# Performance work log

Hardware: AMD Instinct MI355X
Metric: run time of the kernel (lower is better)

## Reference

```python
import jax, jax.numpy as jnp
import numpy as np
from jax import lax


def setup_inputs() -> dict:
    key = jax.random.key(0)
    ks = jax.random.split(key, 6)
    num_u, num_v, num_h, batch = 64, 256, 256, 8192
    # lecun_normal: std = 1/sqrt(fan_in) where fan_in is the last dim
    def lecun(k, shape):
        return jax.random.normal(k, shape, dtype=jnp.float32) * jnp.sqrt(1.0 / shape[1])
    return {
        "u_state": (jax.random.uniform(ks[0], (batch, num_u)) < 0.5).astype(jnp.float32),
        "weights_vu": lecun(ks[1], (num_v, num_u)),
        "weights_hu": lecun(ks[2], (num_h, num_u)),
        "weights_hv": lecun(ks[3], (num_h, num_v)),
        "bias_v": jax.random.normal(ks[4], (num_v,), dtype=jnp.float32) * 0.01,
        "bias_h": jax.random.normal(ks[5], (num_h,), dtype=jnp.float32) * 0.01,
        "therm_steps": 24,
        "size": 8,
    }


def reference(u_state, weights_vu, weights_hu, weights_hv, bias_v, bias_h,
              therm_steps, size):
    """ConditionalRBM.sample: init visible from u, thermalize therm_steps
    Gibbs sweeps, then collect `size` consecutive Gibbs samples."""
    key = jax.random.key(1)

    def bern(k, p):
        # binomial(n=1, p) == bernoulli(p)
        return (jax.random.uniform(k, p.shape) < p).astype(jnp.float32)

    def gibbs_step(v, k):
        k1, k2 = jax.random.split(k)
        ph = jax.nn.sigmoid(v @ weights_hv.T + u_state @ weights_hu.T + bias_h)  # [B,H]
        h = bern(k1, ph)
        pv = jax.nn.sigmoid(h @ weights_hv + u_state @ weights_vu.T + bias_v)    # [B,V]
        return bern(k2, pv)

    ks = jax.random.split(key, therm_steps + size + 1)
    # initial visible state from the conditional prior p(v|u)
    v0 = bern(ks[0], jax.nn.sigmoid(u_state @ weights_vu.T + bias_v))
    # thermalization chain (sequential, loop-carried)
    v_therm, _ = lax.scan(lambda v, k: (gibbs_step(v, k), None), v0, ks[1:1 + therm_steps])
    # sampling chain, stack the `size` samples
    def sample_step(v, k):
        v_new = gibbs_step(v, k)
        return v_new, v_new
    _, samples = lax.scan(sample_step, v_therm, ks[1 + therm_steps:])
    return samples.astype(jnp.uint8)  # [size, B, V]
```

## Files before the change

### kernel.cpp

```cpp
#include <hip/hip_runtime.h>
#include <cstdint>
#include <cstddef>


#pragma clang fp contract(off)

#define BATCH 8192
#define NU 64
#define NF 256
#define BM 64
#define BN 64
#define RTI 16
#define THERM 24
#define NSAMP 8

__host__ __device__ __forceinline__ void tf2x32(uint32_t k0, uint32_t k1,
                                                uint32_t x0, uint32_t x1,
                                                uint32_t* o0, uint32_t* o1) {
  uint32_t ks2 = k0 ^ k1 ^ 0x1BD11BDAu;
  x0 += k0; x1 += k1;
#define TFR(r) { x0 += x1; x1 = (x1 << (r)) | (x1 >> (32 - (r))); x1 ^= x0; }
  TFR(13) TFR(15) TFR(26) TFR(6)
  x0 += k1;  x1 += ks2 + 1u;
  TFR(17) TFR(29) TFR(16) TFR(24)
  x0 += ks2; x1 += k0 + 2u;
  TFR(13) TFR(15) TFR(26) TFR(6)
  x0 += k0;  x1 += k1 + 3u;
  TFR(17) TFR(29) TFR(16) TFR(24)
  x0 += k1;  x1 += ks2 + 4u;
  TFR(13) TFR(15) TFR(26) TFR(6)
  x0 += ks2; x1 += k0 + 5u;
#undef TFR
  *o0 = x0; *o1 = x1;
}

__device__ __forceinline__ float xla_expf(float x) {
  float xc = fminf(x, 88.3762626647950f);
  xc = fmaxf(xc, -88.3762626647949f);
  float fx = floorf(__builtin_fmaf(xc, 1.44269504088896341f, 0.5f));
  float tmp = 0.693359375f * fx;
  float z = -2.12194440e-4f * fx;
  float r = xc - tmp;
  r = r - z;
  z = r * r;
  float y = __builtin_fmaf(r, 1.9875691500e-4f, 1.3981999507e-3f);
  y = __builtin_fmaf(y, r, 8.3334519073e-3f);
  y = __builtin_fmaf(y, r, 4.1665795894e-2f);
  y = __builtin_fmaf(y, r, 1.6666665459e-1f);
  y = __builtin_fmaf(y, r, 5.0000001201e-1f);
  y = __builtin_fmaf(y, z, r);
  y = y + 1.0f;
  int n = (int)fx;
  float p2 = __int_as_float((n + 127) << 23);
  float res = y * p2;
  return fmaxf(res, x);
}

__device__ __forceinline__ float sigmoid_ref(float x) {
  float e = xla_expf(-x);
  return 1.0f / (1.0f + e);
}

__device__ __forceinline__ float bern_sample(uint32_t key0, uint32_t key1,
                                             uint32_t idx, float p) {
  uint32_t b0, b1;
  tf2x32(key0, key1, 0u, idx, &b0, &b1);
  uint32_t bits = b0 ^ b1;
  float u = __uint_as_float((bits >> 9) | 0x3f800000u) - 1.0f;
  return (u < p) ? 1.0f : 0.0f;
}

__global__ void k_transpose(const float* __restrict__ Whv,
                            float* __restrict__ WhvT) {
  int j = threadIdx.x;
  int k = blockIdx.x;
  WhvT[k * NF + j] = Whv[j * NF + k];
}

__global__ __launch_bounds__(256, 2) void k_udot(const float* __restrict__ U,
                                                 const float* __restrict__ W,
                                                 float* __restrict__ out) {
  __shared__ __align__(16) float Ulds[NU * RTI];
  const int j = threadIdx.x;
  const int i0 = blockIdx.x * RTI;
  const int si = j & 15;
  const int sg = j >> 4;
  {
    float4 u4 = *(const float4*)(U + (size_t)(i0 + si) * NU + sg * 4);
    Ulds[(sg * 4 + 0) * RTI + si] = u4.x;
    Ulds[(sg * 4 + 1) * RTI + si] = u4.y;
    Ulds[(sg * 4 + 2) * RTI + si] = u4.z;
    Ulds[(sg * 4 + 3) * RTI + si] = u4.w;
  }
  float wreg[NU];
  const float4* wr4 = (const float4*)(W + (size_t)j * NU);
#pragma unroll
  for (int r = 0; r < NU / 4; ++r) {
    float4 t = wr4[r];
    wreg[4 * r + 0] = t.x; wreg[4 * r + 1] = t.y;
    wreg[4 * r + 2] = t.z; wreg[4 * r + 3] = t.w;
  }
  __syncthreads();
  float acc[RTI];
#pragma unroll
  for (int i = 0; i < RTI; ++i) acc[i] = 0.0f;
#pragma unroll
  for (int kk = 0; kk < NU; ++kk) {
    const float w = wreg[kk];
    const float4 s0 = *(const float4*)(&Ulds[kk * RTI + 0]);
    const float4 s1 = *(const float4*)(&Ulds[kk * RTI + 4]);
    const float4 s2 = *(const float4*)(&Ulds[kk * RTI + 8]);
    const float4 s3 = *(const float4*)(&Ulds[kk * RTI + 12]);
    acc[0]  = __builtin_fmaf(s0.x, w, acc[0]);
    acc[1]  = __builtin_fmaf(s0.y, w, acc[1]);
    acc[2]  = __builtin_fmaf(s0.z, w, acc[2]);
    acc[3]  = __builtin_fmaf(s0.w, w, acc[3]);
    acc[4]  = __builtin_fmaf(s1.x, w, acc[4]);
    acc[5]  = __builtin_fmaf(s1.y, w, acc[5]);
    acc[6]  = __builtin_fmaf(s1.z, w, acc[6]);
    acc[7]  = __builtin_fmaf(s1.w, w, acc[7]);
    acc[8]  = __builtin_fmaf(s2.x, w, acc[8]);
    acc[9]  = __builtin_fmaf(s2.y, w, acc[9]);
    acc[10] = __builtin_fmaf(s2.z, w, acc[10]);
    acc[11] = __builtin_fmaf(s2.w, w, acc[11]);
    acc[12] = __builtin_fmaf(s3.x, w, acc[12]);
    acc[13] = __builtin_fmaf(s3.y, w, acc[13]);
    acc[14] = __builtin_fmaf(s3.z, w, acc[14]);
    acc[15] = __builtin_fmaf(s3.w, w, acc[15]);
  }
#pragma unroll
  for (int i = 0; i < RTI; ++i)
    out[(size_t)(i0 + i) * NF + j] = acc[i];
}

__global__ __launch_bounds__(256) void k_init(const float* __restrict__ uv,
                                              const float* __restrict__ bv,
                                              uint32_t* __restrict__ Vb,
                                              uint32_t key0, uint32_t key1) {
  const int j = threadIdx.x;
  const int i0 = blockIdx.x * RTI;
  const int wv = j >> 6, lane = j & 63;
  const float b = bv[j];
#pragma unroll
  for (int i = 0; i < RTI; ++i) {
    const int row = i0 + i;
    const uint32_t idx = (uint32_t)(row * NF + j);
    const float p = sigmoid_ref(uv[idx] + b);
    const float v = bern_sample(key0, key1, idx, p);
    unsigned long long m = __ballot(v != 0.0f);
    if (lane == 0)
      *(uint2*)(Vb + (size_t)row * 8 + 2 * wv) =
          make_uint2((uint32_t)m, (uint32_t)(m >> 32));
  }
}

__global__ __launch_bounds__(256, 2) void k_phase(
    const uint32_t* __restrict__ Sb, const float* __restrict__ W,
    const float* __restrict__ C, const float* __restrict__ bias,
    uint32_t* __restrict__ Ob, int* __restrict__ smp,
    uint32_t key0, uint32_t key1) {
  __shared__ __align__(16) float Wlds[NF * BN];
  __shared__ __align__(8) uint32_t Smask[BM * 8];
  __shared__ uint32_t Nib[BM * 16];
  const int t  = threadIdx.x;
  const int i0 = (blockIdx.x & 127) * BM;
  const int c0 = (blockIdx.x >> 7) * BN;
  const int rg = t >> 4, cg = t & 15;
  const int jc = c0 + cg * 4;
  const int r0 = i0 + rg * 4;

  {
    const int row = t >> 2, wo = (t & 3) * 2;
    *(uint2*)(&Smask[row * 8 + wo]) =
        *(const uint2*)(Sb + (size_t)(i0 + row) * 8 + wo);
  }
#pragma unroll
  for (int b = 0; b < 4; ++b) {
    float4 tmp0, tmp1, tmp2, tmp3;
    {
      const int f0 = (b * 4 + 0) * 256 + t;
      const int f1 = (b * 4 + 1) * 256 + t;
      const int f2 = (b * 4 + 2) * 256 + t;
      const int f3 = (b * 4 + 3) * 256 + t;
      tmp0 = *(const float4*)(W + (size_t)(f0 >> 4) * NF + c0 + (f0 & 15) * 4);
      tmp1 = *(const float4*)(W + (size_t)(f1 >> 4) * NF + c0 + (f1 & 15) * 4);
      tmp2 = *(const float4*)(W + (size_t)(f2 >> 4) * NF + c0 + (f2 & 15) * 4);
      tmp3 = *(const float4*)(W + (size_t)(f3 >> 4) * NF + c0 + (f3 & 15) * 4);
      *(float4*)(&Wlds[(size_t)(f0 >> 4) * BN + (f0 & 15) * 4]) = tmp0;
      *(float4*)(&Wlds[(size_t)(f1 >> 4) * BN + (f1 & 15) * 4]) = tmp1;
      *(float4*)(&Wlds[(size_t)(f2 >> 4) * BN + (f2 & 15) * 4]) = tmp2;
      *(float4*)(&Wlds[(size_t)(f3 >> 4) * BN + (f3 & 15) * 4]) = tmp3;
    }
  }
  __syncthreads();

  float acc[16];
#pragma unroll
  for (int q = 0; q < 16; ++q) acc[q] = 0.0f;

  const uint32_t* smrow = &Smask[(rg * 4) * 8];

  for (int wi = 0; wi < 8; ++wi) {
    const uint32_t wd0 = smrow[0 * 8 + wi];
    const uint32_t wd1 = smrow[1 * 8 + wi];
    const uint32_t wd2 = smrow[2 * 8 + wi];
    const uint32_t wd3 = smrow[3 * 8 + wi];
    const float* wl = &Wlds[(wi * 32) * BN + cg * 4];
#pragma unroll
    for (int kk = 0; kk < 32; ++kk) {
      const float4 w = *(const float4*)(wl + kk * BN);
      const float s0 = (float)((wd0 >> kk) & 1u);
      const float s1 = (float)((wd1 >> kk) & 1u);
      const float s2 = (float)((wd2 >> kk) & 1u);
      const float s3 = (float)((wd3 >> kk) & 1u);
      acc[0]  = __builtin_fmaf(s0, w.x, acc[0]);
      acc[1]  = __builtin_fmaf(s0, w.y, acc[1]);
      acc[2]  = __builtin_fmaf(s0, w.z, acc[2]);
      acc[3]  = __builtin_fmaf(s0, w.w, acc[3]);
      acc[4]  = __builtin_fmaf(s1, w.x, acc[4]);
      acc[5]  = __builtin_fmaf(s1, w.y, acc[5]);
      acc[6]  = __builtin_fmaf(s1, w.z, acc[6]);
      acc[7]  = __builtin_fmaf(s1, w.w, acc[7]);
      acc[8]  = __builtin_fmaf(s2, w.x, acc[8]);
      acc[9]  = __builtin_fmaf(s2, w.y, acc[9]);
      acc[10] = __builtin_fmaf(s2, w.z, acc[10]);
      acc[11] = __builtin_fmaf(s2, w.w, acc[11]);
      acc[12] = __builtin_fmaf(s3, w.x, acc[12]);
      acc[13] = __builtin_fmaf(s3, w.y, acc[13]);
      acc[14] = __builtin_fmaf(s3, w.z, acc[14]);
      acc[15] = __builtin_fmaf(s3, w.w, acc[15]);
    }
  }

  const float4 b4 = *(const float4*)(bias + jc);
  float vals[16];
#pragma unroll
  for (int ri = 0; ri < 4; ++ri) {
    const int row = r0 + ri;
    const float4 c4 = *(const float4*)(C + (size_t)row * NF + jc);
    const uint32_t idx0 = (uint32_t)(row * NF + jc);
    vals[ri * 4 + 0] = bern_sample(key0, key1, idx0 + 0,
        sigmoid_ref((acc[ri * 4 + 0] + c4.x) + b4.x));
    vals[ri * 4 + 1] = bern_sample(key0, key1, idx0 + 1,
        sigmoid_ref((acc[ri * 4 + 1] + c4.y) + b4.y));
    vals[ri * 4 + 2] = bern_sample(key0, key1, idx0 + 2,
        sigmoid_ref((acc[ri * 4 + 2] + c4.z) + b4.z));
    vals[ri * 4 + 3] = bern_sample(key0, key1, idx0 + 3,
        sigmoid_ref((acc[ri * 4 + 3] + c4.w) + b4.w));
  }

  if (smp) {
#pragma unroll
    for (int ri = 0; ri < 4; ++ri) {
      const int row = r0 + ri;
      int4 o;
      o.x = (vals[ri * 4 + 0] != 0.0f) ? 1 : 0;
      o.y = (vals[ri * 4 + 1] != 0.0f) ? 1 : 0;
      o.z = (vals[ri * 4 + 2] != 0.0f) ? 1 : 0;
      o.w = (vals[ri * 4 + 3] != 0.0f) ? 1 : 0;
      *(int4*)(smp + (size_t)row * NF + jc) = o;
    }
  }

#pragma unroll
  for (int ri = 0; ri < 4; ++ri) {
    uint32_t nb = (vals[ri * 4 + 0] != 0.0f ? 1u : 0u) |
                  (vals[ri * 4 + 1] != 0.0f ? 2u : 0u) |
                  (vals[ri * 4 + 2] != 0.0f ? 4u : 0u) |
                  (vals[ri * 4 + 3] != 0.0f ? 8u : 0u);
    Nib[(rg * 4 + ri) * 16 + cg] = nb;
  }
  __syncthreads();
  if (t < 128) {
    const int row = t >> 1, half = t & 1;
    const uint32_t* nb = &Nib[row * 16 + half * 8];
    uint32_t wrd = nb[0] | (nb[1] << 4) | (nb[2] << 8) | (nb[3] << 12) |
                   (nb[4] << 16) | (nb[5] << 20) | (nb[6] << 24) | (nb[7] << 28);
    Ob[(size_t)(i0 + row) * 8 + (c0 >> 5) + half] = wrd;
  }
}

extern "C" void kernel_launch(void* const* d_in, const int* in_sizes, int n_in,
                              void* d_out, int out_size, void* d_ws, size_t ws_size,
                              hipStream_t stream) {
  const float* u_state = (const float*)d_in[0];
  const float* Wvu     = (const float*)d_in[1];
  const float* Whu     = (const float*)d_in[2];
  const float* Whv     = (const float*)d_in[3];
  const float* bv      = (const float*)d_in[4];
  const float* bh      = (const float*)d_in[5];
  int* out = (int*)d_out;

  float* ws   = (float*)d_ws;
  float* WhvT = ws;
  float* uh   = WhvT + NF * NF;
  float* uv   = uh + (size_t)BATCH * NF;
  uint32_t* Vb = (uint32_t*)(uv + (size_t)BATCH * NF);
  uint32_t* Hb = Vb + (size_t)BATCH * 8;

  uint32_t s0[THERM + NSAMP + 1], s1[THERM + NSAMP + 1];
  for (uint32_t i = 0; i < THERM + NSAMP + 1; ++i)
    tf2x32(0u, 1u, 0u, i, &s0[i], &s1[i]);

  k_transpose<<<NF, NF, 0, stream>>>(Whv, WhvT);
  k_udot<<<BATCH / RTI, NF, 0, stream>>>(u_state, Whu, uh);
  k_udot<<<BATCH / RTI, NF, 0, stream>>>(u_state, Wvu, uv);
  k_init<<<BATCH / RTI, NF, 0, stream>>>(uv, bv, Vb, s0[0], s1[0]);

  const int phase_blocks = (BATCH / BM) * (NF / BN);
  for (int t = 0; t < THERM + NSAMP; ++t) {
    uint32_t kh0, kh1, kv0, kv1;
    tf2x32(s0[1 + t], s1[1 + t], 0u, 0u, &kh0, &kh1);
    tf2x32(s0[1 + t], s1[1 + t], 0u, 1u, &kv0, &kv1);
    int* smp = (t >= THERM) ? out + (size_t)(t - THERM) * BATCH * NF : (int*)nullptr;
    k_phase<<<phase_blocks, NF, 0, stream>>>(Vb, WhvT, uh, bh, Hb, (int*)nullptr, kh0, kh1);
    k_phase<<<phase_blocks, NF, 0, stream>>>(Hb, Whv, uv, bv, Vb, smp, kv0, kv1);
  }
  (void)in_sizes; (void)n_in; (void)out_size; (void)ws_size;
}
```

Before: 1.635 ms.

## Fuse entire Gibbs chain into one persistent kernel with LDS-resident state

Replaces the 64 per-phase launches and the init kernel with a single kernel. Each block owns 16 batch rows for the whole chain and keeps its bit-packed visible and hidden state, the u-projections and the biases in LDS. The weight matrix is streamed through double-buffered LDS chunks using async global_load_lds, and the RNG keys are derived on device. This removes launch overhead and global round-trips of the state, but every block now reads the full 256x256 weight matrix each phase, which raises L2 traffic, and the kernel adds many block-wide barriers.

```diff
diff --git a/kernel.cpp b/kernel.cpp
--- a/kernel.cpp
+++ b/kernel.cpp
@@ -8,11 +8,13 @@
 #define BATCH 8192
 #define NU 64
 #define NF 256
-#define BM 64
-#define BN 64
+#define RPB 16
+#define CH 16
+#define NCH (NF / CH)
 #define RTI 16
 #define THERM 24
 #define NSAMP 8
+#define NSTEP (THERM + NSAMP)
 
 __host__ __device__ __forceinline__ void tf2x32(uint32_t k0, uint32_t k1,
                                                 uint32_t x0, uint32_t x1,
@@ -68,6 +70,12 @@
   uint32_t bits = b0 ^ b1;
   float u = __uint_as_float((bits >> 9) | 0x3f800000u) - 1.0f;
   return (u < p) ? 1.0f : 0.0f;
+}
+
+__device__ __forceinline__ void gld_lds16(const float* g, float* l) {
+  __builtin_amdgcn_global_load_lds(
+      (const __attribute__((address_space(1))) void*)g,
+      (__attribute__((address_space(3))) void*)l, 16, 0, 0);
 }
 
 __global__ void k_transpose(const float* __restrict__ Whv,
@@ -133,150 +141,183 @@
     out[(size_t)(i0 + i) * NF + j] = acc[i];
 }
 
-__global__ __launch_bounds__(256) void k_init(const float* __restrict__ uv,
-                                              const float* __restrict__ bv,
-                                              uint32_t* __restrict__ Vb,
-                                              uint32_t key0, uint32_t key1) {
-  const int j = threadIdx.x;
-  const int i0 = blockIdx.x * RTI;
-  const int wv = j >> 6, lane = j & 63;
-  const float b = bv[j];
-#pragma unroll
-  for (int i = 0; i < RTI; ++i) {
-    const int row = i0 + i;
-    const uint32_t idx = (uint32_t)(row * NF + j);
-    const float p = sigmoid_ref(uv[idx] + b);
-    const float v = bern_sample(key0, key1, idx, p);
-    unsigned long long m = __ballot(v != 0.0f);
-    if (lane == 0)
-      *(uint2*)(Vb + (size_t)row * 8 + 2 * wv) =
-          make_uint2((uint32_t)m, (uint32_t)(m >> 32));
-  }
-}
-
-__global__ __launch_bounds__(256, 2) void k_phase(
-    const uint32_t* __restrict__ Sb, const float* __restrict__ W,
-    const float* __restrict__ C, const float* __restrict__ bias,
-    uint32_t* __restrict__ Ob, int* __restrict__ smp,
-    uint32_t key0, uint32_t key1) {
-  __shared__ __align__(16) float Wlds[NF * BN];
-  __shared__ __align__(8) uint32_t Smask[BM * 8];
-  __shared__ uint32_t Nib[BM * 16];
-  const int t  = threadIdx.x;
-  const int i0 = (blockIdx.x & 127) * BM;
-  const int c0 = (blockIdx.x >> 7) * BN;
-  const int rg = t >> 4, cg = t & 15;
-  const int jc = c0 + cg * 4;
-  const int r0 = i0 + rg * 4;
+__global__ __launch_bounds__(256, 2) void k_chain(
+    const float* __restrict__ Whv, const float* __restrict__ WhvT,
+    const float* __restrict__ uh, const float* __restrict__ uv,
+    const float* __restrict__ bh, const float* __restrict__ bv,
+    int* __restrict__ out) {
+  __shared__ __align__(16) float Wbuf[2][CH * NF];
+  __shared__ __align__(16) float Cu[2][RPB * NF];
+  __shared__ uint32_t bitsL[2][RPB * 8];
+  __shared__ uint32_t nib[RPB * 64];
+  __shared__ float biasL[2][NF];
+  __shared__ uint32_t ksL[66];
+  __shared__ uint32_t keysL[NSTEP * 4];
+
+  const int t = threadIdx.x;
+  const int rowbase = blockIdx.x * RPB;
+  const int rg = t & 3;
+  const int cgg = t >> 2;
+  const int jc = cgg * 4;
 
   {
-    const int row = t >> 2, wo = (t & 3) * 2;
-    *(uint2*)(&Smask[row * 8 + wo]) =
-        *(const uint2*)(Sb + (size_t)(i0 + row) * 8 + wo);
-  }
-#pragma unroll
-  for (int b = 0; b < 4; ++b) {
-    float4 tmp0, tmp1, tmp2, tmp3;
-    {
-      const int f0 = (b * 4 + 0) * 256 + t;
-      const int f1 = (b * 4 + 1) * 256 + t;
-      const int f2 = (b * 4 + 2) * 256 + t;
-      const int f3 = (b * 4 + 3) * 256 + t;
-      tmp0 = *(const float4*)(W + (size_t)(f0 >> 4) * NF + c0 + (f0 & 15) * 4);
-      tmp1 = *(const float4*)(W + (size_t)(f1 >> 4) * NF + c0 + (f1 & 15) * 4);
-      tmp2 = *(const float4*)(W + (size_t)(f2 >> 4) * NF + c0 + (f2 & 15) * 4);
-      tmp3 = *(const float4*)(W + (size_t)(f3 >> 4) * NF + c0 + (f3 & 15) * 4);
-      *(float4*)(&Wlds[(size_t)(f0 >> 4) * BN + (f0 & 15) * 4]) = tmp0;
-      *(float4*)(&Wlds[(size_t)(f1 >> 4) * BN + (f1 & 15) * 4]) = tmp1;
-      *(float4*)(&Wlds[(size_t)(f2 >> 4) * BN + (f2 & 15) * 4]) = tmp2;
-      *(float4*)(&Wlds[(size_t)(f3 >> 4) * BN + (f3 & 15) * 4]) = tmp3;
+    const float4* gu = (const float4*)(uh + (size_t)rowbase * NF);
+    const float4* gv = (const float4*)(uv + (size_t)rowbase * NF);
+    float4* lu = (float4*)Cu[0];
+    float4* lv = (float4*)Cu[1];
+#pragma unroll
+    for (int q = 0; q < 4; ++q) {
+      lu[q * 256 + t] = gu[q * 256 + t];
+      lv[q * 256 + t] = gv[q * 256 + t];
     }
-  }
-  __syncthreads();
-
-  float acc[16];
-#pragma unroll
-  for (int q = 0; q < 16; ++q) acc[q] = 0.0f;
-
-  const uint32_t* smrow = &Smask[(rg * 4) * 8];
-
-  for (int wi = 0; wi < 8; ++wi) {
-    const uint32_t wd0 = smrow[0 * 8 + wi];
-    const uint32_t wd1 = smrow[1 * 8 + wi];
-    const uint32_t wd2 = smrow[2 * 8 + wi];
-    const uint32_t wd3 = smrow[3 * 8 + wi];
-    const float* wl = &Wlds[(wi * 32) * BN + cg * 4];
-#pragma unroll
-    for (int kk = 0; kk < 32; ++kk) {
-      const float4 w = *(const float4*)(wl + kk * BN);
-      const float s0 = (float)((wd0 >> kk) & 1u);
-      const float s1 = (float)((wd1 >> kk) & 1u);
-      const float s2 = (float)((wd2 >> kk) & 1u);
-      const float s3 = (float)((wd3 >> kk) & 1u);
-      acc[0]  = __builtin_fmaf(s0, w.x, acc[0]);
-      acc[1]  = __builtin_fmaf(s0, w.y, acc[1]);
-      acc[2]  = __builtin_fmaf(s0, w.z, acc[2]);
-      acc[3]  = __builtin_fmaf(s0, w.w, acc[3]);
-      acc[4]  = __builtin_fmaf(s1, w.x, acc[4]);
-      acc[5]  = __builtin_fmaf(s1, w.y, acc[5]);
-      acc[6]  = __builtin_fmaf(s1, w.z, acc[6]);
-      acc[7]  = __builtin_fmaf(s1, w.w, acc[7]);
-      acc[8]  = __builtin_fmaf(s2, w.x, acc[8]);
-      acc[9]  = __builtin_fmaf(s2, w.y, acc[9]);
-      acc[10] = __builtin_fmaf(s2, w.z, acc[10]);
-      acc[11] = __builtin_fmaf(s2, w.w, acc[11]);
-      acc[12] = __builtin_fmaf(s3, w.x, acc[12]);
-      acc[13] = __builtin_fmaf(s3, w.y, acc[13]);
-      acc[14] = __builtin_fmaf(s3, w.z, acc[14]);
-      acc[15] = __builtin_fmaf(s3, w.w, acc[15]);
+    biasL[0][t] = bh[t];
+    biasL[1][t] = bv[t];
+    if (t < 33) tf2x32(0u, 1u, 0u, (uint32_t)t, &ksL[2 * t], &ksL[2 * t + 1]);
+  }
+  __syncthreads();
+  if (t < NSTEP) {
+    uint32_t a = ksL[2 * (1 + t)], b2 = ksL[2 * (1 + t) + 1];
+    tf2x32(a, b2, 0u, 0u, &keysL[4 * t + 0], &keysL[4 * t + 1]);
+    tf2x32(a, b2, 0u, 1u, &keysL[4 * t + 2], &keysL[4 * t + 3]);
+  }
+  __syncthreads();
+
+  {
+    const uint32_t k0 = ksL[0], k1 = ksL[1];
+#pragma unroll
+    for (int ri = 0; ri < 4; ++ri) {
+      const int lr = rg * 4 + ri;
+      const int row = rowbase + lr;
+      uint32_t nb = 0;
+#pragma unroll
+      for (int ci = 0; ci < 4; ++ci) {
+        const int j = jc + ci;
+        const float x = Cu[1][lr * NF + j] + biasL[1][j];
+        const float v = bern_sample(k0, k1, (uint32_t)(row * NF + j),
+                                    sigmoid_ref(x));
+        nb |= (v != 0.0f ? 1u : 0u) << ci;
+      }
+      nib[lr * 64 + cgg] = nb;
     }
   }
-
-  const float4 b4 = *(const float4*)(bias + jc);
-  float vals[16];
-#pragma unroll
-  for (int ri = 0; ri < 4; ++ri) {
-    const int row = r0 + ri;
-    const float4 c4 = *(const float4*)(C + (size_t)row * NF + jc);
-    const uint32_t idx0 = (uint32_t)(row * NF + jc);
-    vals[ri * 4 + 0] = bern_sample(key0, key1, idx0 + 0,
-        sigmoid_ref((acc[ri * 4 + 0] + c4.x) + b4.x));
-    vals[ri * 4 + 1] = bern_sample(key0, key1, idx0 + 1,
-        sigmoid_ref((acc[ri * 4 + 1] + c4.y) + b4.y));
-    vals[ri * 4 + 2] = bern_sample(key0, key1, idx0 + 2,
-        sigmoid_ref((acc[ri * 4 + 2] + c4.z) + b4.z));
-    vals[ri * 4 + 3] = bern_sample(key0, key1, idx0 + 3,
-        sigmoid_ref((acc[ri * 4 + 3] + c4.w) + b4.w));
-  }
-
-  if (smp) {
-#pragma unroll
-    for (int ri = 0; ri < 4; ++ri) {
-      const int row = r0 + ri;
-      int4 o;
-      o.x = (vals[ri * 4 + 0] != 0.0f) ? 1 : 0;
-      o.y = (vals[ri * 4 + 1] != 0.0f) ? 1 : 0;
-      o.z = (vals[ri * 4 + 2] != 0.0f) ? 1 : 0;
-      o.w = (vals[ri * 4 + 3] != 0.0f) ? 1 : 0;
-      *(int4*)(smp + (size_t)row * NF + jc) = o;
+  __syncthreads();
+  if (t < 128) {
+    const int lr = t >> 3, wo = t & 7;
+    const uint32_t* nn = &nib[lr * 64 + wo * 8];
+    uint32_t wrd = 0;
+#pragma unroll
+    for (int g = 0; g < 8; ++g) wrd |= nn[g] << (4 * g);
+    bitsL[0][lr * 8 + wo] = wrd;
+  }
+  __syncthreads();
+
+#pragma unroll 1
+  for (int tt = 0; tt < NSTEP; ++tt) {
+#pragma unroll 1
+    for (int ph = 0; ph < 2; ++ph) {
+      const float* M = ph ? Whv : WhvT;
+      const uint32_t* sb = bitsL[ph];
+      uint32_t* db = bitsL[ph ^ 1];
+      const float* Cl = Cu[ph];
+      const float* bl = biasL[ph];
+      const uint32_t k0 = keysL[4 * tt + 2 * ph + 0];
+      const uint32_t k1 = keysL[4 * tt + 2 * ph + 1];
+      int* smp = (ph == 1 && tt >= THERM)
+                     ? out + (size_t)(tt - THERM) * BATCH * NF
+                     : (int*)nullptr;
+
+      float acc[16];
+#pragma unroll
+      for (int q = 0; q < 16; ++q) acc[q] = 0.0f;
+
+#pragma unroll
+      for (int q = 0; q < 4; ++q)
+        gld_lds16(M + (size_t)(q * 256 + t) * 4, &Wbuf[0][(q * 256 + t) * 4]);
+      __syncthreads();
+
+#pragma unroll 1
+      for (int c = 0; c < NCH; ++c) {
+        if (c + 1 < NCH) {
+          const float* src = M + (size_t)(c + 1) * CH * NF;
+          float* dst = Wbuf[(c + 1) & 1];
+#pragma unroll
+          for (int q = 0; q < 4; ++q)
+            gld_lds16(src + (size_t)(q * 256 + t) * 4,
+                      &dst[(q * 256 + t) * 4]);
+        }
+        const int wi = c >> 1;
+        const int hs = (c & 1) * 16;
+        const uint32_t wd0 = sb[(rg * 4 + 0) * 8 + wi] >> hs;
+        const uint32_t wd1 = sb[(rg * 4 + 1) * 8 + wi] >> hs;
+        const uint32_t wd2 = sb[(rg * 4 + 2) * 8 + wi] >> hs;
+        const uint32_t wd3 = sb[(rg * 4 + 3) * 8 + wi] >> hs;
+        const float* wl = &Wbuf[c & 1][jc];
+#pragma unroll
+        for (int kk = 0; kk < CH; ++kk) {
+          const float4 w = *(const float4*)(wl + kk * NF);
+          const float s0 = (float)((wd0 >> kk) & 1u);
+          const float s1 = (float)((wd1 >> kk) & 1u);
+          const float s2 = (float)((wd2 >> kk) & 1u);
+          const float s3 = (float)((wd3 >> kk) & 1u);
+          acc[0]  = __builtin_fmaf(s0, w.x, acc[0]);
+          acc[1]  = __builtin_fmaf(s0, w.y, acc[1]);
+          acc[2]  = __builtin_fmaf(s0, w.z, acc[2]);
+          acc[3]  = __builtin_fmaf(s0, w.w, acc[3]);
+          acc[4]  = __builtin_fmaf(s1, w.x, acc[4]);
+          acc[5]  = __builtin_fmaf(s1, w.y, acc[5]);
+          acc[6]  = __builtin_fmaf(s1, w.z, acc[6]);
+          acc[7]  = __builtin_fmaf(s1, w.w, acc[7]);
+          acc[8]  = __builtin_fmaf(s2, w.x, acc[8]);
+          acc[9]  = __builtin_fmaf(s2, w.y, acc[9]);
+          acc[10] = __builtin_fmaf(s2, w.z, acc[10]);
+          acc[11] = __builtin_fmaf(s2, w.w, acc[11]);
+          acc[12] = __builtin_fmaf(s3, w.x, acc[12]);
+          acc[13] = __builtin_fmaf(s3, w.y, acc[13]);
+          acc[14] = __builtin_fmaf(s3, w.z, acc[14]);
+          acc[15] = __builtin_fmaf(s3, w.w, acc[15]);
+        }
+        __syncthreads();
+      }
+
+      const float4 b4 = *(const float4*)(bl + jc);
+#pragma unroll
+      for (int ri = 0; ri < 4; ++ri) {
+        const int lr = rg * 4 + ri;
+        const int row = rowbase + lr;
+        const float4 c4 = *(const float4*)(Cl + lr * NF + jc);
+        const uint32_t idx0 = (uint32_t)(row * NF + jc);
+        const float v0 = bern_sample(k0, k1, idx0 + 0,
+            sigmoid_ref((acc[ri * 4 + 0] + c4.x) + b4.x));
+        const float v1 = bern_sample(k0, k1, idx0 + 1,
+            sigmoid_ref((acc[ri * 4 + 1] + c4.y) + b4.y));
+        const float v2 = bern_sample(k0, k1, idx0 + 2,
+            sigmoid_ref((acc[ri * 4 + 2] + c4.z) + b4.z));
+        const float v3 = bern_sample(k0, k1, idx0 + 3,
+            sigmoid_ref((acc[ri * 4 + 3] + c4.w) + b4.w));
+        nib[lr * 64 + cgg] = (v0 != 0.0f ? 1u : 0u) |
+                             (v1 != 0.0f ? 2u : 0u) |
+                             (v2 != 0.0f ? 4u : 0u) |
+                             (v3 != 0.0f ? 8u : 0u);
+        if (smp) {
+          int4 o;
+          o.x = (v0 != 0.0f) ? 1 : 0;
+          o.y = (v1 != 0.0f) ? 1 : 0;
+          o.z = (v2 != 0.0f) ? 1 : 0;
+          o.w = (v3 != 0.0f) ? 1 : 0;
+          *(int4*)(smp + (size_t)row * NF + jc) = o;
+        }
+      }
+      __syncthreads();
+      if (t < 128) {
+        const int lr = t >> 3, wo = t & 7;
+        const uint32_t* nn = &nib[lr * 64 + wo * 8];
+        uint32_t wrd = 0;
+#pragma unroll
+        for (int g = 0; g < 8; ++g) wrd |= nn[g] << (4 * g);
+        db[lr * 8 + wo] = wrd;
+      }
+      __syncthreads();
     }
-  }
-
-#pragma unroll
-  for (int ri = 0; ri < 4; ++ri) {
-    uint32_t nb = (vals[ri * 4 + 0] != 0.0f ? 1u : 0u) |
-                  (vals[ri * 4 + 1] != 0.0f ? 2u : 0u) |
-                  (vals[ri * 4 + 2] != 0.0f ? 4u : 0u) |
-                  (vals[ri * 4 + 3] != 0.0f ? 8u : 0u);
-    Nib[(rg * 4 + ri) * 16 + cg] = nb;
-  }
-  __syncthreads();
-  if (t < 128) {
-    const int row = t >> 1, half = t & 1;
-    const uint32_t* nb = &Nib[row * 16 + half * 8];
-    uint32_t wrd = nb[0] | (nb[1] << 4) | (nb[2] << 8) | (nb[3] << 12) |
-                   (nb[4] << 16) | (nb[5] << 20) | (nb[6] << 24) | (nb[7] << 28);
-    Ob[(size_t)(i0 + row) * 8 + (c0 >> 5) + half] = wrd;
   }
 }
 
@@ -295,26 +336,11 @@
   float* WhvT = ws;
   float* uh   = WhvT + NF * NF;
   float* uv   = uh + (size_t)BATCH * NF;
-  uint32_t* Vb = (uint32_t*)(uv + (size_t)BATCH * NF);
-  uint32_t* Hb = Vb + (size_t)BATCH * 8;
-
-  uint32_t s0[THERM + NSAMP + 1], s1[THERM + NSAMP + 1];
-  for (uint32_t i = 0; i < THERM + NSAMP + 1; ++i)
-    tf2x32(0u, 1u, 0u, i, &s0[i], &s1[i]);
 
   k_transpose<<<NF, NF, 0, stream>>>(Whv, WhvT);
   k_udot<<<BATCH / RTI, NF, 0, stream>>>(u_state, Whu, uh);
   k_udot<<<BATCH / RTI, NF, 0, stream>>>(u_state, Wvu, uv);
-  k_init<<<BATCH / RTI, NF, 0, stream>>>(uv, bv, Vb, s0[0], s1[0]);
-
-  const int phase_blocks = (BATCH / BM) * (NF / BN);
-  for (int t = 0; t < THERM + NSAMP; ++t) {
-    uint32_t kh0, kh1, kv0, kv1;
-    tf2x32(s0[1 + t], s1[1 + t], 0u, 0u, &kh0, &kh1);
-    tf2x32(s0[1 + t], s1[1 + t], 0u, 1u, &kv0, &kv1);
-    int* smp = (t >= THERM) ? out + (size_t)(t - THERM) * BATCH * NF : (int*)nullptr;
-    k_phase<<<phase_blocks, NF, 0, stream>>>(Vb, WhvT, uh, bh, Hb, (int*)nullptr, kh0, kh1);
-    k_phase<<<phase_blocks, NF, 0, stream>>>(Hb, Whv, uv, bv, Vb, smp, kv0, kv1);
-  }
+  k_chain<<<BATCH / RPB, NF, 0, stream>>>(Whv, WhvT, uh, uv, bh, bv, out);
+
   (void)in_sizes; (void)n_in; (void)out_size; (void)ws_size;
 }
```

After: 1.655 ms. Within noise of the previous version (+1.2%).
